# Optimization experiments

Measured on AMD Instinct MI355X. Metric: run time of the kernel, lower is better.

## Reference

```python
import jax, jax.numpy as jnp
import numpy as np

N_HEADS = 8
HEAD_DIM = 32
KSIZE = 3
IN_CH = 128
OUT_CH = 256


def setup_inputs() -> dict:
    key = jax.random.key(0)
    k1, k2, k3, k4 = jax.random.split(key, 4)
    x = jax.random.normal(k1, (8, IN_CH, 64, 64), dtype=jnp.float32)
    w_key = jax.random.normal(k2, (N_HEADS * HEAD_DIM, IN_CH), dtype=jnp.float32) * 0.05
    b_key = jax.random.normal(k3, (N_HEADS * HEAD_DIM,), dtype=jnp.float32) * 0.05
    # memory init in torch: uniform in [-1, 1)
    memory = jax.random.uniform(k4, (N_HEADS, HEAD_DIM * KSIZE * KSIZE, OUT_CH // N_HEADS),
                                dtype=jnp.float32) * 2.0 - 1.0
    return {"x": x, "w_key": w_key, "b_key": b_key, "memory": memory}


def _unfold(z, k):
    # z: [b, C, Hp, Wp] padded; returns [b, C*k*k, H*W] with torch.unfold layout
    b, C, Hp, Wp = z.shape
    H, W = Hp - k + 1, Wp - k + 1
    patches = [z[:, :, i:i + H, j:j + W] for i in range(k) for j in range(k)]
    # stack -> [b, C, k*k, H, W]; channel-major like torch unfold (C outer, kh*k+kw inner)
    p = jnp.stack(patches, axis=2)
    return p.reshape(b, C * k * k, H * W)


def reference(x, w_key, b_key, memory):
    b, c_in, H, W = x.shape
    k = KSIZE
    m = N_HEADS
    # 1x1 conv (to_mem_key)
    key_map = jnp.einsum('oi,bihw->bohw', w_key, x) + b_key[None, :, None, None]
    # ZeroPad2d((k//2, k%2, k//2, k%2)) = (left, right, top, bottom)
    pl, pr = k // 2, k % 2
    padded = jnp.pad(key_map, ((0, 0), (0, 0), (pl, pr), (pl, pr)))
    unf = _unfold(padded, k)                      # [b, C*k*k, L], C = m*head_dim
    ckk = unf.shape[1]
    L = unf.shape[2]
    c = ckk // m
    # rearrange 'b (c m) l -> b m c l' (m is the FAST factor, per einops pattern)
    attn = unf.reshape(b, c, m, L).transpose(0, 2, 1, 3)   # [b, m, c, L]
    attn = jax.nn.softmax(attn, axis=2)
    out = jnp.einsum('nki,bnkl->bnil', memory, attn)       # [b, m, head_out, L]
    # rearrange 'b m c (h w) -> b (m c) h w'
    return out.reshape(b, m * out.shape[2], H, W)
```

## Files before the change

### kernel.cpp

```cpp
#include <hip/hip_runtime.h>
#include <hip/hip_bf16.h>

#define B_   8
#define CIN  128
#define CKEY 256
#define NH   8
#define HOUT 32
#define CPH  288
#define HW   4096

#define ESTR   264
#define EROW   (66 * ESTR)
#define E2_BYTES   (4 * EROW * 2)
#define XBUF_BYTES (64 * 136 * 2)
#define SMEM_BYTES (E2_BYTES + XBUF_BYTES)

typedef __attribute__((ext_vector_type(8))) short bf16x8;
typedef __attribute__((ext_vector_type(4))) float f32x4;

__device__ __forceinline__ unsigned bfpack2(float a, float b) {
  __hip_bfloat162 h = __float22bfloat162_rn(float2{a, b});
  unsigned r;
  __builtin_memcpy(&r, &h, 4);
  return r;
}
__device__ __forceinline__ unsigned short f2bf(float f) {
  unsigned u = __builtin_bit_cast(unsigned, f);
  u += 0x7FFFu + ((u >> 16) & 1u);
  return (unsigned short)(u >> 16);
}

__global__ __launch_bounds__(256) void prep_kernel(
    const float* __restrict__ wk, const float* __restrict__ mem,
    unsigned short* __restrict__ wfragP, unsigned short* __restrict__ mfragP)
{
  const int gb = blockIdx.x;
  if (gb < 16) {
    const int idx  = gb * 256 + threadIdx.x;
    const int lane = idx & 63, fi = idx >> 6;
    const int ks = fi & 3, sh = (fi >> 2) & 1, cm = fi >> 3;
    const int li = lane & 15, q = lane >> 4;
    const int och = cm + 8 * (sh * 16 + li);
    const int ic0 = ks * 32 + q * 8;
    unsigned short* dst = wfragP + (size_t)idx * 8;
#pragma unroll
    for (int j = 0; j < 8; ++j) dst[j] = f2bf(wk[och * CIN + ic0 + j]);
  } else {
    const int idx  = (gb - 16) * 256 + threadIdx.x;
    const int lane = idx & 63, fi = idx >> 6;
    const int ib = fi & 1, pm = fi >> 1;
    const int p = pm % 9, m = pm / 9;
    const int li = lane & 15, q = lane >> 4;
    const int i  = ib * 16 + li;
    unsigned short* dst = mfragP + (size_t)idx * 8;
#pragma unroll
    for (int j = 0; j < 8; ++j) {
      const int s = q * 8 + j;
      const int c = ((m - p + 8) & 7) + 8 * s;
      const int t = (9 * c + p) >> 3;
      dst[j] = f2bf(mem[(m * CPH + t) * HOUT + i]);
    }
  }
}

__global__ __launch_bounds__(512, 2) void fused_kernel(
    const float* __restrict__ x, const unsigned short* __restrict__ wfragP,
    const unsigned short* __restrict__ mfragP, const float* __restrict__ bk,
    float* __restrict__ out)
{
  extern __shared__ char smem[];
  unsigned short* e2 = (unsigned short*)smem;
  unsigned*       xdw = (unsigned*)(smem + E2_BYTES);
  float*          tileb = (float*)(smem + E2_BYTES);

  const int tid = threadIdx.x;
  const int bid = blockIdx.x;
  const int b  = bid & 7;
  const int h0 = (bid >> 3) * 2;
  const int lane = tid & 63;
  const int wv = __builtin_amdgcn_readfirstlane(tid >> 6);
  const int li = lane & 15, q = lane >> 4;

  float bias[2][4];
#pragma unroll
  for (int sh = 0; sh < 2; ++sh)
#pragma unroll
    for (int r = 0; r < 4; ++r)
      bias[sh][r] = bk[wv + 8 * (sh * 16 + 4 * q + r)];

  const int spx = tid & 63, sicg = tid >> 6;
  const int sxor = ((spx >> 3) & 7) << 3;

  const bool valid[4] = {h0 - 1 >= 0, true, true, h0 + 2 < 64};
  unsigned pk[4][8];
#pragma unroll
  for (int r = 0; r < 4; ++r) {
    if (!valid[r]) continue;
    const int y = h0 - 1 + r;
    const float* xr = x + (size_t)b * CIN * HW + y * 64 + spx;
#pragma unroll
    for (int r4 = 0; r4 < 4; ++r4) {
      const int ic0 = 4 * sicg + 32 * r4;
      const float v0 = xr[(size_t)(ic0 + 0) * HW];
      const float v1 = xr[(size_t)(ic0 + 1) * HW];
      const float v2 = xr[(size_t)(ic0 + 2) * HW];
      const float v3 = xr[(size_t)(ic0 + 3) * HW];
      pk[r][2 * r4 + 0] = bfpack2(v0, v1);
      pk[r][2 * r4 + 1] = bfpack2(v2, v3);
    }
  }

#pragma unroll
  for (int r = 0; r < 4; r += 3) {
    if (!valid[r]) {
      unsigned* erow = (unsigned*)(e2 + r * EROW);
      for (int d = tid; d < 66 * 132; d += 512) erow[d] = 0x3F803F80u;
    }
  }

#pragma unroll
  for (int rr = 0; rr < 4; ++rr) {
    if (valid[rr]) {
#pragma unroll
      for (int r4 = 0; r4 < 4; ++r4) {
        const int o = (2 * sicg + 16 * r4) ^ sxor;
        *(uint2*)(xdw + spx * 68 + o) = make_uint2(pk[rr][2 * r4], pk[rr][2 * r4 + 1]);
      }
    }
    __syncthreads();
    if (valid[rr]) {
      f32x4 acc[2][4];
#pragma unroll
      for (int sh = 0; sh < 2; ++sh)
#pragma unroll
        for (int pt = 0; pt < 4; ++pt) {
          f32x4 cv; cv[0] = bias[sh][0]; cv[1] = bias[sh][1];
          cv[2] = bias[sh][2]; cv[3] = bias[sh][3];
          acc[sh][pt] = cv;
        }
#pragma unroll
      for (int ks = 0; ks < 4; ++ks) {
        const bf16x8 a0 = *(const bf16x8*)(
            wfragP + ((size_t)(((wv * 2 + 0) * 4 + ks) * 64 + lane)) * 8);
        const bf16x8 a1 = *(const bf16x8*)(
            wfragP + ((size_t)(((wv * 2 + 1) * 4 + ks) * 64 + lane)) * 8);
#pragma unroll
        for (int pt = 0; pt < 4; ++pt) {
          const int px  = pt * 16 + li;
          const int blk = (ks * 16 + q * 4) ^ (((px >> 3) & 7) << 3);
          const bf16x8 bfr = *(const bf16x8*)(xdw + px * 68 + blk);
          acc[0][pt] = __builtin_amdgcn_mfma_f32_16x16x32_bf16(a0, bfr, acc[0][pt], 0, 0, 0);
          acc[1][pt] = __builtin_amdgcn_mfma_f32_16x16x32_bf16(a1, bfr, acc[1][pt], 0, 0, 0);
        }
      }
      unsigned short* erow = e2 + rr * EROW;
#pragma unroll
      for (int sh = 0; sh < 2; ++sh)
#pragma unroll
        for (int pt = 0; pt < 4; ++pt) {
          const float w0 = __expf(acc[sh][pt][0]);
          const float w1 = __expf(acc[sh][pt][1]);
          const float w2 = __expf(acc[sh][pt][2]);
          const float w3 = __expf(acc[sh][pt][3]);
          unsigned short* dst = erow + (pt * 16 + li + 1) * ESTR
                              + wv * 32 + sh * 16 + 4 * q;
          *(uint2*)dst = make_uint2(bfpack2(w0, w1), bfpack2(w2, w3));
        }
      if (tid < 256) {
        const int xcol = (tid & 1) ? 65 : 0;
        ((unsigned*)(erow + xcol * ESTR))[tid >> 1] = 0x3F803F80u;
      }
    }
    __syncthreads();
  }

  const int m = wv;
  const unsigned short* mf = mfragP + (size_t)(m * 9) * 2 * 64 * 8;
  const int4 onesi = make_int4(0x3F803F80, 0x3F803F80, 0x3F803F80, 0x3F803F80);
  const bf16x8 bones = __builtin_bit_cast(bf16x8, onesi);
  float* tw = tileb + wv * (16 * 33);

#pragma unroll
  for (int hh = 0; hh < 2; ++hh) {
    f32x4 acc[4][2], accs[4];
#pragma unroll
    for (int pb = 0; pb < 4; ++pb) {
      acc[pb][0] = {0.f, 0.f, 0.f, 0.f};
      acc[pb][1] = {0.f, 0.f, 0.f, 0.f};
      accs[pb]   = {0.f, 0.f, 0.f, 0.f};
    }
#pragma unroll
    for (int p = 0; p < 9; ++p) {
      const bf16x8 bm0 = *(const bf16x8*)(mf + ((size_t)((p * 2 + 0) * 64 + lane)) * 8);
      const bf16x8 bm1 = *(const bf16x8*)(mf + ((size_t)((p * 2 + 1) * 64 + lane)) * 8);
      const int cm   = (m - p + 8) & 7;
      const int rrow = hh + p / 3;
      const int dxp  = p - 3 * (p / 3);
      const unsigned short* abase = e2 + rrow * EROW + (li + dxp) * ESTR
                                  + cm * 32 + q * 8;
#pragma unroll
      for (int pb = 0; pb < 4; ++pb) {
        const bf16x8 af = *(const bf16x8*)(abase + pb * 16 * ESTR);
        acc[pb][0] = __builtin_amdgcn_mfma_f32_16x16x32_bf16(af, bm0, acc[pb][0], 0, 0, 0);
        acc[pb][1] = __builtin_amdgcn_mfma_f32_16x16x32_bf16(af, bm1, acc[pb][1], 0, 0, 0);
        accs[pb]   = __builtin_amdgcn_mfma_f32_16x16x32_bf16(af, bones, accs[pb], 0, 0, 0);
      }
    }
    float* ob = out + ((size_t)(b * CKEY + m * HOUT)) * HW + (h0 + hh) * 64;
#pragma unroll
    for (int pb = 0; pb < 4; ++pb) {
#pragma unroll
      for (int r = 0; r < 4; ++r) {
        const float inv = 1.0f / accs[pb][r];
        tw[(q * 4 + r) * 33 + li]      = acc[pb][0][r] * inv;
        tw[(q * 4 + r) * 33 + 16 + li] = acc[pb][1][r] * inv;
      }
#pragma unroll
      for (int s2 = 0; s2 < 8; ++s2) {
        const int i = s2 * 4 + q;
        ob[(size_t)i * HW + pb * 16 + li] = tw[li * 33 + i];
      }
    }
  }
}

extern "C" void kernel_launch(void* const* d_in, const int* in_sizes, int n_in,
                              void* d_out, int out_size, void* d_ws, size_t ws_size,
                              hipStream_t stream) {
  const float* x   = (const float*)d_in[0];
  const float* wk  = (const float*)d_in[1];
  const float* bk  = (const float*)d_in[2];
  const float* mem = (const float*)d_in[3];

  unsigned short* wfragP = (unsigned short*)d_ws;
  unsigned short* mfragP = (unsigned short*)((char*)d_ws + 65536);

  (void)hipFuncSetAttribute((const void*)fused_kernel,
                            hipFuncAttributeMaxDynamicSharedMemorySize, SMEM_BYTES);

  prep_kernel<<<dim3(52), dim3(256), 0, stream>>>(wk, mem, wfragP, mfragP);
  fused_kernel<<<dim3(256), dim3(512), SMEM_BYTES, stream>>>(
      x, wfragP, mfragP, bk, (float*)d_out);
}
```

Before: 94.47 us.

## Fold weight prep into fused kernel and swap MFMA operands for direct stores

Removes the separate prep kernel: each wave now loads and converts its key-weight and memory fragments to bf16 registers straight from the fp32 inputs inside the fused kernel. The second GEMM's MFMA operands are swapped so the accumulator layout matches the output (channel rows, pixel columns). Results can then be written directly to global memory without the LDS transpose tile, and the normalizer reads a single accumulator lane. This removes a kernel launch and LDS traffic at the cost of more registers (9x2 memory fragments plus 8 weight fragments held live) and redundant per-block conversion work.

```diff
diff --git a/kernel.cpp b/kernel.cpp
--- a/kernel.cpp
+++ b/kernel.cpp
@@ -18,60 +18,21 @@
 typedef __attribute__((ext_vector_type(8))) short bf16x8;
 typedef __attribute__((ext_vector_type(4))) float f32x4;
 
-__device__ __forceinline__ unsigned bfpack2(float a, float b) {
+static __device__ __forceinline__ unsigned bfpack2(float a, float b) {
   __hip_bfloat162 h = __float22bfloat162_rn(float2{a, b});
   unsigned r;
   __builtin_memcpy(&r, &h, 4);
   return r;
 }
-__device__ __forceinline__ unsigned short f2bf(float f) {
-  unsigned u = __builtin_bit_cast(unsigned, f);
-  u += 0x7FFFu + ((u >> 16) & 1u);
-  return (unsigned short)(u >> 16);
-}
-
-__global__ __launch_bounds__(256) void prep_kernel(
-    const float* __restrict__ wk, const float* __restrict__ mem,
-    unsigned short* __restrict__ wfragP, unsigned short* __restrict__ mfragP)
-{
-  const int gb = blockIdx.x;
-  if (gb < 16) {
-    const int idx  = gb * 256 + threadIdx.x;
-    const int lane = idx & 63, fi = idx >> 6;
-    const int ks = fi & 3, sh = (fi >> 2) & 1, cm = fi >> 3;
-    const int li = lane & 15, q = lane >> 4;
-    const int och = cm + 8 * (sh * 16 + li);
-    const int ic0 = ks * 32 + q * 8;
-    unsigned short* dst = wfragP + (size_t)idx * 8;
-#pragma unroll
-    for (int j = 0; j < 8; ++j) dst[j] = f2bf(wk[och * CIN + ic0 + j]);
-  } else {
-    const int idx  = (gb - 16) * 256 + threadIdx.x;
-    const int lane = idx & 63, fi = idx >> 6;
-    const int ib = fi & 1, pm = fi >> 1;
-    const int p = pm % 9, m = pm / 9;
-    const int li = lane & 15, q = lane >> 4;
-    const int i  = ib * 16 + li;
-    unsigned short* dst = mfragP + (size_t)idx * 8;
-#pragma unroll
-    for (int j = 0; j < 8; ++j) {
-      const int s = q * 8 + j;
-      const int c = ((m - p + 8) & 7) + 8 * s;
-      const int t = (9 * c + p) >> 3;
-      dst[j] = f2bf(mem[(m * CPH + t) * HOUT + i]);
-    }
-  }
-}
 
 __global__ __launch_bounds__(512, 2) void fused_kernel(
-    const float* __restrict__ x, const unsigned short* __restrict__ wfragP,
-    const unsigned short* __restrict__ mfragP, const float* __restrict__ bk,
+    const float* __restrict__ x, const float* __restrict__ wk,
+    const float* __restrict__ mem, const float* __restrict__ bk,
     float* __restrict__ out)
 {
   extern __shared__ char smem[];
   unsigned short* e2 = (unsigned short*)smem;
   unsigned*       xdw = (unsigned*)(smem + E2_BYTES);
-  float*          tileb = (float*)(smem + E2_BYTES);
 
   const int tid = threadIdx.x;
   const int bid = blockIdx.x;
@@ -110,6 +71,43 @@
     }
   }
 
+  bf16x8 wf[2][4];
+#pragma unroll
+  for (int sh = 0; sh < 2; ++sh)
+#pragma unroll
+    for (int ks = 0; ks < 4; ++ks) {
+      const int och = wv + 8 * (sh * 16 + li);
+      const float* src = wk + (size_t)och * CIN + ks * 32 + q * 8;
+      const float4 v0 = *(const float4*)(src);
+      const float4 v1 = *(const float4*)(src + 4);
+      const int4 piv = make_int4(bfpack2(v0.x, v0.y), bfpack2(v0.z, v0.w),
+                                 bfpack2(v1.x, v1.y), bfpack2(v1.z, v1.w));
+      wf[sh][ks] = __builtin_bit_cast(bf16x8, piv);
+    }
+
+  bf16x8 mfr[9][2];
+#pragma unroll
+  for (int p = 0; p < 9; ++p) {
+    const int cb = (wv - p + 8) & 7;
+#pragma unroll
+    for (int ib = 0; ib < 2; ++ib) {
+      const int i = ib * 16 + li;
+      unsigned pr[4];
+#pragma unroll
+      for (int jj = 0; jj < 4; ++jj) {
+        const int s0 = q * 8 + 2 * jj;
+        const int c0 = cb + 8 * s0;
+        const int c1 = cb + 8 * (s0 + 1);
+        const int t0 = (9 * c0 + p) >> 3;
+        const int t1 = (9 * c1 + p) >> 3;
+        const float f0 = mem[((size_t)wv * CPH + t0) * HOUT + i];
+        const float f1 = mem[((size_t)wv * CPH + t1) * HOUT + i];
+        pr[jj] = bfpack2(f0, f1);
+      }
+      mfr[p][ib] = __builtin_bit_cast(bf16x8, make_int4(pr[0], pr[1], pr[2], pr[3]));
+    }
+  }
+
 #pragma unroll
   for (int r = 0; r < 4; r += 3) {
     if (!valid[r]) {
@@ -140,10 +138,8 @@
         }
 #pragma unroll
       for (int ks = 0; ks < 4; ++ks) {
-        const bf16x8 a0 = *(const bf16x8*)(
-            wfragP + ((size_t)(((wv * 2 + 0) * 4 + ks) * 64 + lane)) * 8);
-        const bf16x8 a1 = *(const bf16x8*)(
-            wfragP + ((size_t)(((wv * 2 + 1) * 4 + ks) * 64 + lane)) * 8);
+        const bf16x8 a0 = wf[0][ks];
+        const bf16x8 a1 = wf[1][ks];
 #pragma unroll
         for (int pt = 0; pt < 4; ++pt) {
           const int px  = pt * 16 + li;
@@ -175,10 +171,8 @@
   }
 
   const int m = wv;
-  const unsigned short* mf = mfragP + (size_t)(m * 9) * 2 * 64 * 8;
   const int4 onesi = make_int4(0x3F803F80, 0x3F803F80, 0x3F803F80, 0x3F803F80);
   const bf16x8 bones = __builtin_bit_cast(bf16x8, onesi);
-  float* tw = tileb + wv * (16 * 33);
 
 #pragma unroll
   for (int hh = 0; hh < 2; ++hh) {
@@ -191,8 +185,8 @@
     }
 #pragma unroll
     for (int p = 0; p < 9; ++p) {
-      const bf16x8 bm0 = *(const bf16x8*)(mf + ((size_t)((p * 2 + 0) * 64 + lane)) * 8);
-      const bf16x8 bm1 = *(const bf16x8*)(mf + ((size_t)((p * 2 + 1) * 64 + lane)) * 8);
+      const bf16x8 bm0 = mfr[p][0];
+      const bf16x8 bm1 = mfr[p][1];
       const int cm   = (m - p + 8) & 7;
       const int rrow = hh + p / 3;
       const int dxp  = p - 3 * (p / 3);
@@ -201,25 +195,21 @@
 #pragma unroll
       for (int pb = 0; pb < 4; ++pb) {
         const bf16x8 af = *(const bf16x8*)(abase + pb * 16 * ESTR);
-        acc[pb][0] = __builtin_amdgcn_mfma_f32_16x16x32_bf16(af, bm0, acc[pb][0], 0, 0, 0);
-        acc[pb][1] = __builtin_amdgcn_mfma_f32_16x16x32_bf16(af, bm1, acc[pb][1], 0, 0, 0);
-        accs[pb]   = __builtin_amdgcn_mfma_f32_16x16x32_bf16(af, bones, accs[pb], 0, 0, 0);
+        acc[pb][0] = __builtin_amdgcn_mfma_f32_16x16x32_bf16(bm0, af, acc[pb][0], 0, 0, 0);
+        acc[pb][1] = __builtin_amdgcn_mfma_f32_16x16x32_bf16(bm1, af, acc[pb][1], 0, 0, 0);
+        accs[pb]   = __builtin_amdgcn_mfma_f32_16x16x32_bf16(bones, af, accs[pb], 0, 0, 0);
       }
     }
     float* ob = out + ((size_t)(b * CKEY + m * HOUT)) * HW + (h0 + hh) * 64;
 #pragma unroll
     for (int pb = 0; pb < 4; ++pb) {
-#pragma unroll
-      for (int r = 0; r < 4; ++r) {
-        const float inv = 1.0f / accs[pb][r];
-        tw[(q * 4 + r) * 33 + li]      = acc[pb][0][r] * inv;
-        tw[(q * 4 + r) * 33 + 16 + li] = acc[pb][1][r] * inv;
-      }
-#pragma unroll
-      for (int s2 = 0; s2 < 8; ++s2) {
-        const int i = s2 * 4 + q;
-        ob[(size_t)i * HW + pb * 16 + li] = tw[li * 33 + i];
-      }
+      const float inv = 1.0f / accs[pb][0];
+#pragma unroll
+      for (int n = 0; n < 2; ++n)
+#pragma unroll
+        for (int r = 0; r < 4; ++r)
+          ob[(size_t)(n * 16 + 4 * q + r) * HW + pb * 16 + li] =
+              acc[pb][n][r] * inv;
     }
   }
 }
@@ -231,14 +221,11 @@
   const float* wk  = (const float*)d_in[1];
   const float* bk  = (const float*)d_in[2];
   const float* mem = (const float*)d_in[3];
-
-  unsigned short* wfragP = (unsigned short*)d_ws;
-  unsigned short* mfragP = (unsigned short*)((char*)d_ws + 65536);
+  (void)d_ws; (void)ws_size;
 
   (void)hipFuncSetAttribute((const void*)fused_kernel,
                             hipFuncAttributeMaxDynamicSharedMemorySize, SMEM_BYTES);
 
-  prep_kernel<<<dim3(52), dim3(256), 0, stream>>>(wk, mem, wfragP, mfragP);
   fused_kernel<<<dim3(256), dim3(512), SMEM_BYTES, stream>>>(
-      x, wfragP, mfragP, bk, (float*)d_out);
+      x, wk, mem, bk, (float*)d_out);
 }
```

New measurement: 110.9 us. 17.4% more time.
